# Performance work log

Measured on AMD Instinct MI355X. Metric: run time of the kernel, lower is better.

The kernel has to match this reference:

```python
import jax, jax.numpy as jnp
import numpy as np

INTERVAL = 0.02

def setup_inputs() -> dict:
    key = jax.random.key(0)
    ks = jax.random.split(key, 10)
    B, N, D, F = 8, 256, 64, 64
    return {
        "rbf_0": jax.random.normal(ks[0], (B, N, N, D), jnp.float32),
        "rbf_d": jax.random.normal(ks[1], (B, N, N, D), jnp.float32),
        "Q0_w": jax.random.normal(ks[2], (F, D), jnp.float32) * 0.1,
        "Q0_b": jax.random.normal(ks[3], (F,), jnp.float32) * 0.1,
        "Q_w": jax.random.normal(ks[4], (F, D), jnp.float32) * 0.1,
        "Q_b": jax.random.normal(ks[5], (F,), jnp.float32) * 0.1,
        "R0_w": jax.random.normal(ks[6], (F, D), jnp.float32) * 0.1,
        "R0_b": jax.random.normal(ks[7], (F,), jnp.float32) * 0.1,
        "R_w": jax.random.normal(ks[8], (F, D), jnp.float32) * 0.1,
        "R_b": jax.random.normal(ks[9], (F,), jnp.float32) * 0.1,
    }

def _linear(x, w, b):
    # x: [..., D], w: [F, D], b: [F] -> [..., F]
    return jnp.einsum('...d,fd->...f', x, w) + b

def reference(rbf_0, rbf_d, Q0_w, Q0_b, Q_w, Q_b, R0_w, R0_b, R_w, R_b):
    q_0 = _linear(rbf_0, Q0_w, Q0_b)   # [B, N, N, F]
    q = _linear(rbf_d, Q_w, Q_b)       # [B, N, N, F]
    r_0 = _linear(rbf_0, R0_w, R0_b)   # [B, N, N, F]
    r = _linear(rbf_d, R_w, R_b)       # [B, N, N, F]
    # 3-index correlator: contract over i and f
    C = jnp.einsum('bnif,bijf->bnj', q_0 * q, r_0 * r) * INTERVAL
    return C
```

## Files before the change

kernel.cpp:

```cpp
#include <hip/hip_runtime.h>
#include <hip/hip_bf16.h>


typedef __bf16 bf16x8 __attribute__((ext_vector_type(8)));
typedef float  f32x4  __attribute__((ext_vector_type(4)));
typedef int    i32x4  __attribute__((ext_vector_type(4)));
typedef unsigned short u16;
typedef u16    u16x8  __attribute__((ext_vector_type(8)));

static __device__ __forceinline__ __bf16 f2bf(float x) {
  union { __hip_bfloat16 h; __bf16 b; } u;
  u.h = __float2bfloat16(x);
  return u.b;
}
static __device__ __forceinline__ u16 f2bfu(float x) {
  union { __hip_bfloat16 h; u16 s; } u;
  u.h = __float2bfloat16(x);
  return u.s;
}
static __device__ __forceinline__ float bfu2f(u16 s) {
  union { unsigned int u; float f; } v;
  v.u = ((unsigned int)s) << 16;
  return v.f;
}

__global__ __launch_bounds__(256, 3) void k_phase1(
    const float* __restrict__ rbf0, const float* __restrict__ rbfd,
    const float* __restrict__ Q0w, const float* __restrict__ Q0b,
    const float* __restrict__ Qw,  const float* __restrict__ Qb,
    const float* __restrict__ R0w, const float* __restrict__ R0b,
    const float* __restrict__ Rw,  const float* __restrict__ Rb,
    u16* __restrict__ Aout, u16* __restrict__ Bout)
{
  __shared__ __align__(16) float ldsA[2][2048];
  __shared__ __align__(16) float ldsB[2][2048];

  const int tid  = threadIdx.x;
  const int lane = tid & 63;
  const int wave = tid >> 6;
  const int fr   = lane & 15;
  const int kg   = lane >> 4;
  const int role = wave >> 1;
  const int s    = wave & 1;

  const float* W0 = role ? R0w : Q0w;
  const float* W1 = role ? Rw  : Qw;
  const float* B0 = role ? R0b : Q0b;
  const float* B1 = role ? Rb  : Qb;
  u16* __restrict__ Out = role ? Bout : Aout;

  bf16x8 wf0[2][4], wf1[2][4];
#pragma unroll
  for (int kt = 0; kt < 2; ++kt)
#pragma unroll
    for (int ft = 0; ft < 4; ++ft) {
      const float* p0 = W0 + (ft * 16 + fr) * 64 + kt * 32 + kg * 8;
      const float* p1 = W1 + (ft * 16 + fr) * 64 + kt * 32 + kg * 8;
      f32x4 a = *(const f32x4*)p0, b = *(const f32x4*)(p0 + 4);
      f32x4 c = *(const f32x4*)p1, d = *(const f32x4*)(p1 + 4);
      bf16x8 w0v, w1v;
#pragma unroll
      for (int j = 0; j < 4; ++j) {
        w0v[j] = f2bf(a[j]); w0v[j + 4] = f2bf(b[j]);
        w1v[j] = f2bf(c[j]); w1v[j + 4] = f2bf(d[j]);
      }
      wf0[kt][ft] = w0v; wf1[kt][ft] = w1v;
    }

  u16x8 pb0[2], pb1[2];
#pragma unroll
  for (int ft = 0; ft < 4; ++ft)
#pragma unroll
    for (int r = 0; r < 4; ++r) {
      int idx = ft * 4 + r;
      pb0[idx >> 3][idx & 7] = f2bfu(B0[ft * 16 + kg * 4 + r]);
      pb1[idx >> 3][idx & 7] = f2bfu(B1[ft * 16 + kg * 4 + r]);
    }

  const int g0 = tid, g1 = 256 + tid;
  const int w0c = ((g0 >> 4) << 4) | ((g0 & 15) ^ ((g0 >> 4) & 15));
  const int w1c = ((g1 >> 4) << 4) | ((g1 & 15) ^ ((g1 >> 4) & 15));

  const int NBT = 16384;
  const int gstride = gridDim.x;
  int bt = blockIdx.x;

  f32x4 v0a, v0b, v1a, v1b;
  {
    const float* p0 = rbf0 + (size_t)bt * 2048;
    const float* p1 = rbfd + (size_t)bt * 2048;
    v0a = *(const f32x4*)(p0 + tid * 4);
    v0b = *(const f32x4*)(p0 + 1024 + tid * 4);
    v1a = *(const f32x4*)(p1 + tid * 4);
    v1b = *(const f32x4*)(p1 + 1024 + tid * 4);
  }

  const int NIT = NBT / 2048;
  for (int it = 0; it < NIT; ++it) {
    const int set = it & 1;
    const int cbt = bt;

    *(f32x4*)&ldsA[set][w0c * 4] = v0a;
    *(f32x4*)&ldsA[set][w1c * 4] = v0b;
    *(f32x4*)&ldsB[set][w0c * 4] = v1a;
    *(f32x4*)&ldsB[set][w1c * 4] = v1b;

    int btn = bt + gstride;
    int btl = (btn < NBT) ? btn : 0;
    {
      const float* p0 = rbf0 + (size_t)btl * 2048;
      const float* p1 = rbfd + (size_t)btl * 2048;
      v0a = *(const f32x4*)(p0 + tid * 4);
      v0b = *(const f32x4*)(p0 + 1024 + tid * 4);
      v1a = *(const f32x4*)(p1 + tid * 4);
      v1b = *(const f32x4*)(p1 + 1024 + tid * 4);
    }

    asm volatile("s_waitcnt lgkmcnt(0)" ::: "memory");
    __builtin_amdgcn_s_barrier();
    __builtin_amdgcn_sched_barrier(0);

    const int row = s * 16 + fr;
    f32x4 ra[4], rb[4];
#pragma unroll
    for (int kt = 0; kt < 2; ++kt)
#pragma unroll
      for (int h = 0; h < 2; ++h) {
        int c = kt * 8 + kg * 2 + h;
        int chunk = (row << 4) | (c ^ fr);
        ra[kt * 2 + h] = *(const f32x4*)&ldsA[set][chunk * 4];
        rb[kt * 2 + h] = *(const f32x4*)&ldsB[set][chunk * 4];
      }

    bf16x8 x0f[2], xdf[2];
#pragma unroll
    for (int kt = 0; kt < 2; ++kt)
#pragma unroll
      for (int j = 0; j < 4; ++j) {
        x0f[kt][j]     = f2bf(ra[kt * 2][j]);
        x0f[kt][j + 4] = f2bf(ra[kt * 2 + 1][j]);
        xdf[kt][j]     = f2bf(rb[kt * 2][j]);
        xdf[kt][j + 4] = f2bf(rb[kt * 2 + 1][j]);
      }

    f32x4 acc0[4], acc1[4];
#pragma unroll
    for (int ft = 0; ft < 4; ++ft)
#pragma unroll
      for (int r = 0; r < 4; ++r) {
        int idx = ft * 4 + r;
        acc0[ft][r] = bfu2f(pb0[idx >> 3][idx & 7]);
        acc1[ft][r] = bfu2f(pb1[idx >> 3][idx & 7]);
      }

#pragma unroll
    for (int kt = 0; kt < 2; ++kt)
#pragma unroll
      for (int ft = 0; ft < 4; ++ft) {
        acc0[ft] = __builtin_amdgcn_mfma_f32_16x16x32_bf16(wf0[kt][ft], x0f[kt], acc0[ft], 0, 0, 0);
        acc1[ft] = __builtin_amdgcn_mfma_f32_16x16x32_bf16(wf1[kt][ft], xdf[kt], acc1[ft], 0, 0, 0);
      }

    u16x8 o0, o1;
#pragma unroll
    for (int ft = 0; ft < 4; ++ft)
#pragma unroll
      for (int r = 0; r < 4; ++r) {
        int idx = ft * 4 + r;
        float v = acc0[ft][r] * acc1[ft][r];
        if (idx < 8) o0[idx & 7] = f2bfu(v); else o1[idx & 7] = f2bfu(v);
      }
    u16* dst = Out + ((size_t)(cbt * 32 + s * 16 + fr)) * 64 + kg * 16;
    *(u16x8*)dst       = o0;
    *(u16x8*)(dst + 8) = o1;

    bt = btl;
  }
}

__global__ __launch_bounds__(256, 2) void k_phase2(
    const u16* __restrict__ A, const u16* __restrict__ Bm,
    float* __restrict__ C)
{
  __shared__ __align__(16) u16 Alds[128 * 64];
  __shared__ __align__(16) u16 Blds[128 * 64];

  const int tid  = threadIdx.x;
  const int lane = tid & 63;
  const int wave = tid >> 6;
  const int fr   = lane & 15;
  const int kg   = lane >> 4;

  const int bid = blockIdx.x;
  const int kc = bid & 15;
  const int jt = (bid >> 4) & 1;
  const int nt = (bid >> 5) & 1;
  const int b  = bid >> 6;
  const int n0 = nt * 128, j0 = jt * 128;
  const int wr = wave >> 1, wc = wave & 1;

  const u16* Ab = A  + (size_t)b * 4194304;
  const u16* Bb = Bm + (size_t)b * 4194304;

  f32x4 acc[4][4];
#pragma unroll
  for (int mt = 0; mt < 4; ++mt)
#pragma unroll
    for (int nn = 0; nn < 4; ++nn) {
      acc[mt][nn][0] = 0.f; acc[mt][nn][1] = 0.f; acc[mt][nn][2] = 0.f; acc[mt][nn][3] = 0.f;
    }

  for (int ii = 0; ii < 16; ++ii) {
    const int i = kc * 16 + ii;

    i32x4 va[4], vb[4];
#pragma unroll
    for (int rep = 0; rep < 4; ++rep) {
      int c = tid + rep * 256;
      int row = c >> 3, ch = c & 7;
      va[rep] = *(const i32x4*)(Ab + (size_t)(n0 + row) * 16384 + (size_t)i * 64 + ch * 8);
      vb[rep] = *(const i32x4*)(Bb + (size_t)i * 16384 + (size_t)(j0 + row) * 64 + ch * 8);
    }
    __syncthreads();
#pragma unroll
    for (int rep = 0; rep < 4; ++rep) {
      int c = tid + rep * 256;
      int row = c >> 3, ch = c & 7;
      int sw = ch ^ (row & 7);
      *(i32x4*)&Alds[row * 64 + sw * 8] = va[rep];
      *(i32x4*)&Blds[row * 64 + sw * 8] = vb[rep];
    }
    __syncthreads();

#pragma unroll
    for (int ks = 0; ks < 2; ++ks) {
      bf16x8 af[4], bfv[4];
#pragma unroll
      for (int mt = 0; mt < 4; ++mt) {
        int row = wr * 64 + mt * 16 + fr;
        int sw = (ks * 4 + kg) ^ (row & 7);
        af[mt] = *(const bf16x8*)&Alds[row * 64 + sw * 8];
      }
#pragma unroll
      for (int nn = 0; nn < 4; ++nn) {
        int row = wc * 64 + nn * 16 + fr;
        int sw = (ks * 4 + kg) ^ (row & 7);
        bfv[nn] = *(const bf16x8*)&Blds[row * 64 + sw * 8];
      }
#pragma unroll
      for (int mt = 0; mt < 4; ++mt)
#pragma unroll
        for (int nn = 0; nn < 4; ++nn)
          acc[mt][nn] = __builtin_amdgcn_mfma_f32_16x16x32_bf16(af[mt], bfv[nn], acc[mt][nn], 0, 0, 0);
    }
  }

  float* Cb = C + ((size_t)b << 16);
#pragma unroll
  for (int mt = 0; mt < 4; ++mt)
#pragma unroll
    for (int nn = 0; nn < 4; ++nn)
#pragma unroll
      for (int r = 0; r < 4; ++r) {
        int n = n0 + wr * 64 + mt * 16 + kg * 4 + r;
        int j = j0 + wc * 64 + nn * 16 + fr;
        atomicAdd(&Cb[n * 256 + j], acc[mt][nn][r] * 0.02f);
      }
}

extern "C" void kernel_launch(void* const* d_in, const int* in_sizes, int n_in,
                              void* d_out, int out_size, void* d_ws, size_t ws_size,
                              hipStream_t stream)
{
  const float* rbf0 = (const float*)d_in[0];
  const float* rbfd = (const float*)d_in[1];
  const float* Q0w  = (const float*)d_in[2];
  const float* Q0b  = (const float*)d_in[3];
  const float* Qw   = (const float*)d_in[4];
  const float* Qb   = (const float*)d_in[5];
  const float* R0w  = (const float*)d_in[6];
  const float* R0b  = (const float*)d_in[7];
  const float* Rw   = (const float*)d_in[8];
  const float* Rb   = (const float*)d_in[9];
  float* out = (float*)d_out;

  u16* Abuf = (u16*)d_ws;
  u16* Bbuf = Abuf + (size_t)33554432;

  hipMemsetAsync(d_out, 0, (size_t)out_size * sizeof(float), stream);
  hipLaunchKernelGGL(k_phase1, dim3(2048), dim3(256), 0, stream,
                     rbf0, rbfd, Q0w, Q0b, Qw, Qb, R0w, R0b, Rw, Rb, Abuf, Bbuf);
  hipLaunchKernelGGL(k_phase2, dim3(512), dim3(256), 0, stream, Abuf, Bbuf, out);
}
```

Before: 137.2 us.

## Load phase1 inputs directly to LDS with triple-buffered async pipeline

Replaces the register-staged global loads followed by LDS stores with global_load_lds direct-to-LDS transfers, using a 3-stage LDS ring that keeps two tiles in flight. The 8-iteration loop is fully unrolled, with explicit vmcnt waits tuned per iteration. This aims to remove the VGPR staging and ds_write traffic and to hide more memory latency in the bandwidth-bound projection phase. It raises LDS use to 48KB per block, which may cut occupancy below the 3-block launch bound, and it depends on hand-counted vmcnt values, which must also account for the output stores.

```diff
diff --git a/kernel.cpp b/kernel.cpp
--- a/kernel.cpp
+++ b/kernel.cpp
@@ -22,6 +22,11 @@
   union { unsigned int u; float f; } v;
   v.u = ((unsigned int)s) << 16;
   return v.f;
+}
+static __device__ __forceinline__ void gload16(const float* gsrc, float* ldst) {
+  __builtin_amdgcn_global_load_lds(
+      (const __attribute__((address_space(1))) void*)gsrc,
+      (__attribute__((address_space(3))) void*)ldst, 16, 0, 0);
 }
 
 __global__ __launch_bounds__(256, 3) void k_phase1(
@@ -32,8 +37,7 @@
     const float* __restrict__ Rw,  const float* __restrict__ Rb,
     u16* __restrict__ Aout, u16* __restrict__ Bout)
 {
-  __shared__ __align__(16) float ldsA[2][2048];
-  __shared__ __align__(16) float ldsB[2][2048];
+  __shared__ __align__(16) float lds[3][2][2048];
 
   const int tid  = threadIdx.x;
   const int lane = tid & 63;
@@ -78,104 +82,105 @@
     }
 
   const int g0 = tid, g1 = 256 + tid;
-  const int w0c = ((g0 >> 4) << 4) | ((g0 & 15) ^ ((g0 >> 4) & 15));
-  const int w1c = ((g1 >> 4) << 4) | ((g1 & 15) ^ ((g1 >> 4) & 15));
-
-  const int NBT = 16384;
-  const int gstride = gridDim.x;
-  int bt = blockIdx.x;
-
-  f32x4 v0a, v0b, v1a, v1b;
-  {
-    const float* p0 = rbf0 + (size_t)bt * 2048;
-    const float* p1 = rbfd + (size_t)bt * 2048;
-    v0a = *(const f32x4*)(p0 + tid * 4);
-    v0b = *(const f32x4*)(p0 + 1024 + tid * 4);
-    v1a = *(const f32x4*)(p1 + tid * 4);
-    v1b = *(const f32x4*)(p1 + 1024 + tid * 4);
-  }
-
-  const int NIT = NBT / 2048;
-  for (int it = 0; it < NIT; ++it) {
-    const int set = it & 1;
-    const int cbt = bt;
-
-    *(f32x4*)&ldsA[set][w0c * 4] = v0a;
-    *(f32x4*)&ldsA[set][w1c * 4] = v0b;
-    *(f32x4*)&ldsB[set][w0c * 4] = v1a;
-    *(f32x4*)&ldsB[set][w1c * 4] = v1b;
-
-    int btn = bt + gstride;
-    int btl = (btn < NBT) ? btn : 0;
-    {
-      const float* p0 = rbf0 + (size_t)btl * 2048;
-      const float* p1 = rbfd + (size_t)btl * 2048;
-      v0a = *(const f32x4*)(p0 + tid * 4);
-      v0b = *(const f32x4*)(p0 + 1024 + tid * 4);
-      v1a = *(const f32x4*)(p1 + tid * 4);
-      v1b = *(const f32x4*)(p1 + 1024 + tid * 4);
-    }
-
-    asm volatile("s_waitcnt lgkmcnt(0)" ::: "memory");
-    __builtin_amdgcn_s_barrier();
-    __builtin_amdgcn_sched_barrier(0);
-
-    const int row = s * 16 + fr;
-    f32x4 ra[4], rb[4];
-#pragma unroll
-    for (int kt = 0; kt < 2; ++kt)
-#pragma unroll
-      for (int h = 0; h < 2; ++h) {
-        int c = kt * 8 + kg * 2 + h;
-        int chunk = (row << 4) | (c ^ fr);
-        ra[kt * 2 + h] = *(const f32x4*)&ldsA[set][chunk * 4];
-        rb[kt * 2 + h] = *(const f32x4*)&ldsB[set][chunk * 4];
-      }
-
-    bf16x8 x0f[2], xdf[2];
-#pragma unroll
-    for (int kt = 0; kt < 2; ++kt)
-#pragma unroll
-      for (int j = 0; j < 4; ++j) {
-        x0f[kt][j]     = f2bf(ra[kt * 2][j]);
-        x0f[kt][j + 4] = f2bf(ra[kt * 2 + 1][j]);
-        xdf[kt][j]     = f2bf(rb[kt * 2][j]);
-        xdf[kt][j + 4] = f2bf(rb[kt * 2 + 1][j]);
-      }
-
-    f32x4 acc0[4], acc1[4];
-#pragma unroll
-    for (int ft = 0; ft < 4; ++ft)
-#pragma unroll
-      for (int r = 0; r < 4; ++r) {
-        int idx = ft * 4 + r;
-        acc0[ft][r] = bfu2f(pb0[idx >> 3][idx & 7]);
-        acc1[ft][r] = bfu2f(pb1[idx >> 3][idx & 7]);
-      }
-
-#pragma unroll
-    for (int kt = 0; kt < 2; ++kt)
-#pragma unroll
-      for (int ft = 0; ft < 4; ++ft) {
-        acc0[ft] = __builtin_amdgcn_mfma_f32_16x16x32_bf16(wf0[kt][ft], x0f[kt], acc0[ft], 0, 0, 0);
-        acc1[ft] = __builtin_amdgcn_mfma_f32_16x16x32_bf16(wf1[kt][ft], xdf[kt], acc1[ft], 0, 0, 0);
-      }
-
-    u16x8 o0, o1;
-#pragma unroll
-    for (int ft = 0; ft < 4; ++ft)
-#pragma unroll
-      for (int r = 0; r < 4; ++r) {
-        int idx = ft * 4 + r;
-        float v = acc0[ft][r] * acc1[ft][r];
-        if (idx < 8) o0[idx & 7] = f2bfu(v); else o1[idx & 7] = f2bfu(v);
-      }
-    u16* dst = Out + ((size_t)(cbt * 32 + s * 16 + fr)) * 64 + kg * 16;
-    *(u16x8*)dst       = o0;
-    *(u16x8*)(dst + 8) = o1;
-
-    bt = btl;
-  }
+  const int c0 = ((g0 >> 4) << 4) | ((g0 & 15) ^ ((g0 >> 4) & 15));
+  const int c1 = ((g1 >> 4) << 4) | ((g1 & 15) ^ ((g1 >> 4) & 15));
+  const int f0 = c0 * 4, f1 = c1 * 4;
+  const int d0 = wave * 256, d1 = (wave + 4) * 256;
+
+  const int bt0 = blockIdx.x;
+
+#define S1_ISSUE(IT, SET)                                              \
+  {                                                                    \
+    const float* b0_ = rbf0 + (size_t)(bt0 + (IT) * 2048) * 2048;      \
+    const float* b1_ = rbfd + (size_t)(bt0 + (IT) * 2048) * 2048;      \
+    gload16(b0_ + f0, &lds[SET][0][d0]);                               \
+    gload16(b0_ + f1, &lds[SET][0][d1]);                               \
+    gload16(b1_ + f0, &lds[SET][1][d0]);                               \
+    gload16(b1_ + f1, &lds[SET][1][d1]);                               \
+  }
+
+#define S1_COMPUTE(IT, SET)                                            \
+  {                                                                    \
+    const int row = s * 16 + fr;                     \
+    f32x4 ra[4], rb[4];                                                \
+    _Pragma("unroll")                                                  \
+    for (int kt = 0; kt < 2; ++kt)                                     \
+      _Pragma("unroll")                                                \
+      for (int h = 0; h < 2; ++h) {                                    \
+        int c = kt * 8 + kg * 2 + h;                                   \
+        int chunk = (row << 4) | (c ^ fr);                             \
+        ra[kt * 2 + h] = *(const f32x4*)&lds[SET][0][chunk * 4];       \
+        rb[kt * 2 + h] = *(const f32x4*)&lds[SET][1][chunk * 4];       \
+      }                                                                \
+    bf16x8 x0f[2], xdf[2];                                             \
+    _Pragma("unroll")                                                  \
+    for (int kt = 0; kt < 2; ++kt)                                     \
+      _Pragma("unroll")                                                \
+      for (int j = 0; j < 4; ++j) {                                    \
+        x0f[kt][j]     = f2bf(ra[kt * 2][j]);                          \
+        x0f[kt][j + 4] = f2bf(ra[kt * 2 + 1][j]);                      \
+        xdf[kt][j]     = f2bf(rb[kt * 2][j]);                          \
+        xdf[kt][j + 4] = f2bf(rb[kt * 2 + 1][j]);                      \
+      }                                                                \
+    f32x4 acc0[4], acc1[4];                                            \
+    _Pragma("unroll")                                                  \
+    for (int ft = 0; ft < 4; ++ft)                                     \
+      _Pragma("unroll")                                                \
+      for (int r = 0; r < 4; ++r) {                                    \
+        int idx = ft * 4 + r;                                          \
+        acc0[ft][r] = bfu2f(pb0[idx >> 3][idx & 7]);                   \
+        acc1[ft][r] = bfu2f(pb1[idx >> 3][idx & 7]);                   \
+      }                                                                \
+    _Pragma("unroll")                                                  \
+    for (int kt = 0; kt < 2; ++kt)                                     \
+      _Pragma("unroll")                                                \
+      for (int ft = 0; ft < 4; ++ft) {                                 \
+        acc0[ft] = __builtin_amdgcn_mfma_f32_16x16x32_bf16(            \
+            wf0[kt][ft], x0f[kt], acc0[ft], 0, 0, 0);                  \
+        acc1[ft] = __builtin_amdgcn_mfma_f32_16x16x32_bf16(            \
+            wf1[kt][ft], xdf[kt], acc1[ft], 0, 0, 0);                  \
+      }                                                                \
+    u16x8 o0, o1;                                                      \
+    _Pragma("unroll")                                                  \
+    for (int ft = 0; ft < 4; ++ft)                                     \
+      _Pragma("unroll")                                                \
+      for (int r = 0; r < 4; ++r) {                                    \
+        int idx = ft * 4 + r;                                          \
+        float v = acc0[ft][r] * acc1[ft][r];                           \
+        if (idx < 8) o0[idx & 7] = f2bfu(v); else o1[idx & 7] = f2bfu(v); \
+      }                                                                \
+    u16* dst = Out + ((size_t)((bt0 + (IT) * 2048) * 32 + s * 16 + fr)) * 64 + kg * 16; \
+    *(u16x8*)dst       = o0;                                           \
+    *(u16x8*)(dst + 8) = o1;                                           \
+  }
+
+#define S1_ITER(IT, NWAIT, DO_ISSUE)                                   \
+  {                                                                    \
+    if (DO_ISSUE) S1_ISSUE((IT) + 2, ((IT) + 2) % 3);                  \
+    asm volatile("s_waitcnt vmcnt(" #NWAIT ")" ::: "memory");          \
+    __builtin_amdgcn_s_barrier();                                      \
+    __builtin_amdgcn_sched_barrier(0);                                 \
+    S1_COMPUTE(IT, (IT) % 3);                                          \
+    asm volatile("s_waitcnt lgkmcnt(0)" ::: "memory");                 \
+    __builtin_amdgcn_s_barrier();                                      \
+    __builtin_amdgcn_sched_barrier(0);                                 \
+  }
+
+  S1_ISSUE(0, 0);
+  S1_ISSUE(1, 1);
+
+  S1_ITER(0,  8, 1);
+  S1_ITER(1, 10, 1);
+  S1_ITER(2, 12, 1);
+  S1_ITER(3, 12, 1);
+  S1_ITER(4, 12, 1);
+  S1_ITER(5, 12, 1);
+  S1_ITER(6,  8, 0);
+  S1_ITER(7,  4, 0);
+
+#undef S1_ITER
+#undef S1_COMPUTE
+#undef S1_ISSUE
 }
 
 __global__ __launch_bounds__(256, 2) void k_phase2(
```

After: 142.1 us. +3.6%, slower.
